# Performance work log

Measured on AMD Instinct MI355X. Metric: run time of the kernel, lower is better.

The kernel has to match this reference:

```python
import jax, jax.numpy as jnp
import numpy as np

N_GRAPH = 100000
N_CAND = 1000
N_EDGES = 3200000
F_IN = 32


def _param(k, shape):
    return jax.random.normal(k, shape, dtype=jnp.float32) * 0.1


def setup_inputs() -> dict:
    key = jax.random.key(0)
    ks = jax.random.split(key, 20)
    inp = {
        "x": jax.random.normal(ks[0], (N_GRAPH, F_IN), dtype=jnp.float32),
        "candidate_set": jax.random.normal(ks[1], (N_CAND, F_IN), dtype=jnp.float32),
        "edge_index": jax.random.randint(ks[2], (2, N_EDGES), 0, N_GRAPH, dtype=jnp.int32),
        # GCN stack 32 -> 16 -> 24 -> 32
        "W1": _param(ks[3], (F_IN, 16)), "b1": jnp.zeros((16,), jnp.float32),
        "W2": _param(ks[4], (16, 24)),   "b2": jnp.zeros((24,), jnp.float32),
        "W3": _param(ks[5], (24, 32)),   "b3": jnp.zeros((32,), jnp.float32),
        # start-node MLP: 32 -> 16 -> 1
        "Ws1": _param(ks[6], (32, 16)), "bs1": jnp.zeros((16,), jnp.float32),
        "Ws2": _param(ks[7], (16, 1)),  "bs2": jnp.zeros((1,), jnp.float32),
        # end-node MLP: 32 -> 24 -> 1
        "We1": _param(ks[8], (32, 24)), "be1": jnp.zeros((24,), jnp.float32),
        "We2": _param(ks[9], (24, 1)),  "be2": jnp.zeros((1,), jnp.float32),
    }
    return inp


def _relu6(v):
    return jnp.clip(v, 0.0, 6.0)


def _gcn(h, row, col, dinv, W, b, N):
    # PyG GCNConv: h @ W, then D^-1/2 (A+I) D^-1/2 aggregation, then + bias
    h = h @ W
    norm = (dinv[row] * dinv[col])[:, None]
    return jax.ops.segment_sum(h[row] * norm, col, num_segments=N) + b


def reference(x, candidate_set, edge_index, W1, b1, W2, b2, W3, b3,
              Ws1, bs1, Ws2, bs2, We1, be1, We2, be2):
    n_graph = x.shape[0]
    h = jnp.concatenate([x, candidate_set], axis=0)  # [N, F_IN]
    N = h.shape[0]
    sl = jnp.arange(N, dtype=edge_index.dtype)
    row = jnp.concatenate([edge_index[0], sl])  # self-loops appended
    col = jnp.concatenate([edge_index[1], sl])
    deg = jax.ops.segment_sum(jnp.ones(row.shape[0], h.dtype), col, num_segments=N)
    dinv = 1.0 / jnp.sqrt(deg)  # deg >= 1 thanks to self-loops

    for W, b in ((W1, b1), (W2, b2), (W3, b3)):
        h = _gcn(h, row, col, dinv, W, b, N)  # [N, 32] at the end

    # start-node head: softmax over nodes (dim 0)
    start_probs = jax.nn.softmax(_relu6(h @ Ws1 + bs1) @ Ws2 + bs2, axis=0)  # [N,1]
    mask = jnp.ones_like(start_probs).at[n_graph:].set(0.0)  # zero out candidates
    start_probs = start_probs * mask
    start_probs = jnp.where(start_probs == 0.0, 1e-10, start_probs)
    start_probs = start_probs.squeeze()  # [N]
    start_node = jax.random.categorical(jax.random.key(42), jnp.log(start_probs))

    # end-node head
    end_probs = jax.nn.softmax(_relu6(h @ We1 + be1) @ We2 + be2, axis=0)  # [N,1]
    end_probs = end_probs.at[start_node].set(0.0)
    end_probs = jnp.where(end_probs == 0.0, 1e-10, end_probs)
    end_probs = end_probs.squeeze()  # [N]
    end_node = jax.random.categorical(jax.random.key(43), jnp.log(end_probs))

    new_edge = jnp.stack([start_node, end_node]).astype(edge_index.dtype)[:, None]
    edge_index_new = jnp.concatenate([edge_index, new_edge], axis=1)
    return (h, start_probs, end_probs, start_node, end_node, edge_index_new)
```

## Files before the change

kernel.cpp:

```cpp
#include <hip/hip_runtime.h>
#include <math.h>

#define TPB 256
#define BNODES 256
#define EPB 8192
#define SENT (-1)
#define MAXBKT 512
#define STAGE_CAP 14144

typedef _Float16 h8 __attribute__((ext_vector_type(8)));
typedef _Float16 hf;


__device__ __forceinline__ float jax_gumbel(unsigned key, unsigned i) {
  unsigned x0 = 0u, x1 = i;
  unsigned ks0 = 0u, ks1 = key, ks2 = key ^ 0x1BD11BDAu;
  x0 += ks0; x1 += ks1;
#define TFR(r) { x0 += x1; x1 = (x1 << (r)) | (x1 >> (32 - (r))); x1 ^= x0; }
  TFR(13) TFR(15) TFR(26) TFR(6)
  x0 += ks1; x1 += ks2 + 1u;
  TFR(17) TFR(29) TFR(16) TFR(24)
  x0 += ks2; x1 += ks0 + 2u;
  TFR(13) TFR(15) TFR(26) TFR(6)
  x0 += ks0; x1 += ks1 + 3u;
  TFR(17) TFR(29) TFR(16) TFR(24)
  x0 += ks1; x1 += ks2 + 4u;
  TFR(13) TFR(15) TFR(26) TFR(6)
  x0 += ks2; x1 += ks0 + 5u;
#undef TFR
  unsigned bits = x0 ^ x1;
  float f = __uint_as_float((bits >> 9) | 0x3f800000u) - 1.0f;
  float u = (f == 0.0f) ? 1.17549435e-38f : f;
  return -logf(-logf(u));
}

__global__ void hist_k(const int* __restrict__ col, int* __restrict__ hist,
                       int ne, int nbkt, int nblk) {
  __shared__ int h[1024];
  int t = threadIdx.x;
  for (int i = t; i < nbkt; i += TPB) h[i] = 0;
  __syncthreads();
  int base = blockIdx.x * EPB;
#pragma unroll
  for (int k = 0; k < EPB / TPB; k++) {
    int idx = base + k * TPB + t;
    if (idx < ne) atomicAdd(&h[col[idx] >> 8], 1);
  }
  __syncthreads();
  for (int i = t; i < nbkt; i += TPB) hist[(size_t)i * nblk + blockIdx.x] = h[i];
}

__global__ void breal_k(const int* __restrict__ hist, int* __restrict__ breal, int nblk) {
  int bkt = blockIdx.x;
  int t = threadIdx.x;
  int s = 0;
  for (int b = t; b < nblk; b += TPB) s += hist[(size_t)bkt * nblk + b];
  __shared__ int red[TPB];
  red[t] = s; __syncthreads();
  for (int st = 128; st > 0; st >>= 1) { if (t < st) red[t] += red[t + st]; __syncthreads(); }
  if (t == 0) breal[bkt] = red[0];
}

template <int PAD>
__global__ void scan1_k(const int* __restrict__ a, int* __restrict__ bsums, int n) {
  int t = threadIdx.x;
  int base = blockIdx.x * 1024 + t * 4;
  int s = 0;
#pragma unroll
  for (int k = 0; k < 4; k++) {
    int i = base + k;
    if (i < n) { int v = a[i]; if (PAD) v = (v + 15) & ~15; s += v; }
  }
  __shared__ int red[TPB];
  red[t] = s; __syncthreads();
  for (int st = 128; st > 0; st >>= 1) { if (t < st) red[t] += red[t + st]; __syncthreads(); }
  if (t == 0) bsums[blockIdx.x] = red[0];
}

__global__ void scan_single_k(int* a, int m) {
  __shared__ int sc[TPB];
  int t = threadIdx.x;
  int v[4]; int s = 0;
#pragma unroll
  for (int k = 0; k < 4; k++) { int i = t * 4 + k; v[k] = (i < m) ? a[i] : 0; s += v[k]; }
  sc[t] = s; __syncthreads();
  for (int off = 1; off < TPB; off <<= 1) {
    int add = (t >= off) ? sc[t - off] : 0;
    __syncthreads();
    sc[t] += add;
    __syncthreads();
  }
  int excl = sc[t] - s;
#pragma unroll
  for (int k = 0; k < 4; k++) { int i = t * 4 + k; if (i < m) a[i] = excl; excl += v[k]; }
  if (t == TPB - 1) a[m] = excl;
}

template <int PAD>
__global__ void scan3_k(const int* __restrict__ a, const int* __restrict__ bsums,
                        int* __restrict__ outp, int n, int nb) {
  int t = threadIdx.x;
  int base = blockIdx.x * 1024 + t * 4;
  int v[4]; int tsum = 0;
#pragma unroll
  for (int k = 0; k < 4; k++) {
    int vv = 0;
    if (base + k < n) { vv = a[base + k]; if (PAD) vv = (vv + 15) & ~15; }
    v[k] = vv; tsum += vv;
  }
  __shared__ int sc[TPB];
  sc[t] = tsum; __syncthreads();
  for (int off = 1; off < TPB; off <<= 1) {
    int add = (t >= off) ? sc[t - off] : 0;
    __syncthreads();
    sc[t] += add;
    __syncthreads();
  }
  int excl = sc[t] - tsum + bsums[blockIdx.x];
#pragma unroll
  for (int k = 0; k < 4; k++) { if (base + k < n) outp[base + k] = excl; excl += v[k]; }
  if (blockIdx.x == 0 && t == 0) outp[n] = bsums[nb];
}

__global__ void __launch_bounds__(TPB, 1)
bscatter_k(const int* __restrict__ row, const int* __restrict__ col,
           const int* __restrict__ histP, int* __restrict__ pairs,
           float* __restrict__ e0, float* __restrict__ e1,
           int ne, int nbkt, int nblk) {
  __shared__ int sbase[MAXBKT], lofs[MAXBKT], lcur[MAXBKT], lsz[MAXBKT];
  __shared__ int ssc[TPB];
  __shared__ int stage[STAGE_CAP];
  int t = threadIdx.x;
  int b = blockIdx.x;
  int i0 = 2 * t, i1 = 2 * t + 1;
  int g0 = 0, L0 = 0, g1 = 0, L1 = 0;
  if (i0 < nbkt) { size_t f = (size_t)i0 * nblk + b; g0 = histP[f]; L0 = histP[f + 1] - g0; }
  if (i1 < nbkt) { size_t f = (size_t)i1 * nblk + b; g1 = histP[f]; L1 = histP[f + 1] - g1; }
  int s = L0 + L1;
  ssc[t] = s; __syncthreads();
  for (int off = 1; off < TPB; off <<= 1) {
    int add = (t >= off) ? ssc[t - off] : 0;
    __syncthreads();
    ssc[t] += add;
    __syncthreads();
  }
  int excl = ssc[t] - s;
  if (i0 < nbkt) { sbase[i0] = g0; lofs[i0] = excl; lcur[i0] = excl; lsz[i0] = L0; }
  if (i1 < nbkt) { sbase[i1] = g1; lofs[i1] = excl + L0; lcur[i1] = excl + L0; lsz[i1] = L1; }
  __syncthreads();
  int base0 = b * EPB;
#pragma unroll
  for (int k = 0; k < EPB / TPB; k++) {
    int idx = base0 + k * TPB + t;
    if (idx < ne) {
      int c = col[idx];
      int r = row[idx];
      int p = atomicAdd(&lcur[c >> 8], 1);
      stage[p] = (r << 8) | (c & 255);
      e0[idx] = (float)r;
      e1[idx] = (float)c;
    }
  }
  __syncthreads();
  for (int i = t; i < nbkt; i += TPB) {
    int en = lcur[i], pe = lofs[i] + lsz[i];
    for (int p = en; p < pe; p++) stage[p] = SENT;
  }
  __syncthreads();
  int4* gp = (int4*)pairs;
  const int4* sp = (const int4*)stage;
  for (int i = t; i < nbkt; i += TPB) {
    int gb = sbase[i] >> 2, lb = lofs[i] >> 2, m = lsz[i] >> 2;
    for (int q = 0; q < m; q++) gp[gb + q] = sp[lb + q];
  }
}

__global__ void bbuild_k(const int* __restrict__ pairs, const int* __restrict__ histP,
                         const int* __restrict__ bbase, int nblk, int* __restrict__ rp,
                         float* __restrict__ dinv, int* __restrict__ csr, int n, int ne) {
  int bkt = blockIdx.x;
  int lo = bkt << 8;
  int t = threadIdx.x;
  int pstart = histP[(size_t)bkt * nblk];
  int pend   = histP[(size_t)(bkt + 1) * nblk];
  int rbase  = bbase[bkt];
  __shared__ int cnt[BNODES], sc[BNODES], pos[BNODES];
  cnt[t] = 0; __syncthreads();
  for (int p = pstart + t; p < pend; p += TPB) {
    int e = pairs[p];
    if (e >= 0) atomicAdd(&cnt[e & 255], 1);
  }
  __syncthreads();
  int own = cnt[t];
  sc[t] = own; __syncthreads();
  for (int off = 1; off < BNODES; off <<= 1) {
    int add = (t >= off) ? sc[t - off] : 0;
    __syncthreads();
    sc[t] += add;
    __syncthreads();
  }
  int excl = sc[t] - own;
  if (lo + t < n) {
    rp[lo + t] = rbase + excl;
    dinv[lo + t] = 1.0f / sqrtf((float)(own + 1));
  }
  pos[t] = rbase + excl;
  __syncthreads();
  for (int p = pstart + t; p < pend; p += TPB) {
    int e = pairs[p];
    if (e >= 0) {
      int q = atomicAdd(&pos[e & 255], 1);
      csr[q] = e >> 8;
    }
  }
  if (bkt == 0 && t == 0) rp[n] = ne;
}

__global__ void prep_k(const float* __restrict__ W2, const float* __restrict__ W3,
                       const float* __restrict__ b1, const float* __restrict__ b2,
                       float* __restrict__ W23, float* __restrict__ bvA, float* __restrict__ bvB) {
  int t = threadIdx.x;
  for (int idx = t; idx < 512; idx += TPB) {
    int i = idx >> 5, j = idx & 31;
    float s = 0.f;
    for (int k = 0; k < 24; k++) s += W2[i * 24 + k] * W3[k * 32 + j];
    W23[idx] = s;
  }
  __syncthreads();
  if (t < 32) {
    float sA = 0.f;
    for (int i = 0; i < 16; i++) sA += b1[i] * W23[i * 32 + t];
    bvA[t] = sA;
    float sB = 0.f;
    for (int k = 0; k < 24; k++) sB += b2[k] * W3[k * 32 + t];
    bvB[t] = sB;
  }
}

__global__ void gemm16h_k(const float* __restrict__ A, const float* __restrict__ A2, int nsplit,
                          const float* __restrict__ W, const float* __restrict__ dinv,
                          hf* __restrict__ out, int n) {
  constexpr int FIN = 32, FOUT = 16, FP = 16;
  constexpr int NODES = TPB / FP;
  __shared__ float Ws[FIN * FOUT];
  __shared__ float Hs[NODES * (FIN + 1)];
  int t = threadIdx.x;
  int base = blockIdx.x * NODES;
  for (int i = t; i < FIN * FOUT; i += TPB) Ws[i] = W[i];
  for (int i = t; i < NODES * FIN; i += TPB) {
    int nl = i / FIN, k = i - nl * FIN;
    int g = base + nl;
    float v = 0.f;
    if (g < n) v = (g < nsplit) ? A[(size_t)g * FIN + k] : A2[(size_t)(g - nsplit) * FIN + k];
    Hs[nl * (FIN + 1) + k] = v;
  }
  __syncthreads();
  int nl = t / FP, j = t % FP;
  int g = base + nl;
  if (g < n) {
    float acc = 0.f;
#pragma unroll
    for (int k = 0; k < FIN; k++) acc += Hs[nl * (FIN + 1) + k] * Ws[k * FOUT + j];
    out[(size_t)g * FOUT + j] = (hf)(acc * dinv[g]);
  }
}

__global__ void agghs_k(const h8* __restrict__ ts, const int* __restrict__ csr,
                        const int* __restrict__ rp, const float* __restrict__ dinv,
                        const float* __restrict__ sin_, float* __restrict__ u_out,
                        float* __restrict__ us_out, h8* __restrict__ outv, int n) {
  int wave = blockIdx.x * (TPB / 64) + (threadIdx.x >> 6);
  int lane = threadIdx.x & 63;
  int j = lane & 1;
  int grp = (lane >> 1) & 3;
  int nl = lane >> 3;
  int c = wave * 8 + nl;
  bool valid = (c < n);
  float acc[8] = {0.f, 0.f, 0.f, 0.f, 0.f, 0.f, 0.f, 0.f};
  float accS = 0.f;
  if (valid) {
    int s = rp[c], e = rp[c + 1];
    int ch0 = s >> 2, ch1 = (e + 3) >> 2;
    int nch = ch1 - ch0;
    int k0 = ch0 + ((nch * grp) >> 2);
    int k1 = ch0 + ((nch * (grp + 1)) >> 2);
    for (int ch = k0; ch < k1; ch++) {
      int base = ch << 2;
      int4 e4 = *(const int4*)(csr + base);
      bool b0 = (base     >= s) & (base     < e);
      bool b1 = (base + 1 >= s) & (base + 1 < e);
      bool b2 = (base + 2 >= s) & (base + 2 < e);
      bool b3 = (base + 3 >= s) & (base + 3 < e);
      int r0 = b0 ? e4.x : 0;
      int r1 = b1 ? e4.y : 0;
      int r2 = b2 ? e4.z : 0;
      int r3 = b3 ? e4.w : 0;
      float m0 = b0 ? 1.f : 0.f, m1 = b1 ? 1.f : 0.f;
      float m2 = b2 ? 1.f : 0.f, m3 = b3 ? 1.f : 0.f;
      h8 v0 = ts[(r0 << 1) | j];
      h8 v1 = ts[(r1 << 1) | j];
      h8 v2 = ts[(r2 << 1) | j];
      h8 v3 = ts[(r3 << 1) | j];
      float sA = sin_[j ? r2 : r0];
      float sB = sin_[j ? r3 : r1];
      accS += sA * (j ? m2 : m0) + sB * (j ? m3 : m1);
#pragma unroll
      for (int k = 0; k < 8; k++)
        acc[k] += m0 * (float)v0[k] + m1 * (float)v1[k] + m2 * (float)v2[k] + m3 * (float)v3[k];
    }
  }
  accS += __shfl_xor(accS, 1, 64);
#pragma unroll
  for (int off = 2; off <= 4; off <<= 1) {
#pragma unroll
    for (int k = 0; k < 8; k++) acc[k] += __shfl_xor(acc[k], off, 64);
    accS += __shfl_xor(accS, off, 64);
  }
  if (valid && grp == 0) {
    h8 self = ts[(c << 1) | j];
    float d = dinv[c];
    float scl = d * d;
    h8 o;
#pragma unroll
    for (int k = 0; k < 8; k++) o[k] = (hf)(scl * (acc[k] + (float)self[k]));
    outv[(c << 1) | j] = o;
    if (j == 0) {
      float u = d * (accS + sin_[c]);
      u_out[c] = u;
      if (us_out) us_out[c] = u * d;
    }
  }
}

__global__ void agghc_k(const h8* __restrict__ ts, const int* __restrict__ csr,
                        const int* __restrict__ rp, const float* __restrict__ dinv,
                        const float* __restrict__ a1, const float* __restrict__ a2,
                        const float* __restrict__ W23, const float* __restrict__ bvA,
                        const float* __restrict__ bvB, const float* __restrict__ b3,
                        float* __restrict__ out, int n) {
  __shared__ float Ws[512], vA[32], vB[32], vb[32];
  __shared__ float t3s[32][17];
  int t = threadIdx.x;
  for (int i = t; i < 512; i += TPB) Ws[i] = W23[i];
  if (t < 32) { vA[t] = bvA[t]; vB[t] = bvB[t]; vb[t] = b3[t]; }
  int wave = t >> 6;
  int lane = t & 63;
  int j = lane & 1;
  int grp = (lane >> 1) & 3;
  int nl = lane >> 3;
  int nlb = wave * 8 + nl;
  int c = blockIdx.x * 32 + nlb;
  bool valid = (c < n);
  float acc[8] = {0.f, 0.f, 0.f, 0.f, 0.f, 0.f, 0.f, 0.f};
  if (valid) {
    int s = rp[c], e = rp[c + 1];
    int ch0 = s >> 2, ch1 = (e + 3) >> 2;
    int nch = ch1 - ch0;
    int k0 = ch0 + ((nch * grp) >> 2);
    int k1 = ch0 + ((nch * (grp + 1)) >> 2);
    for (int ch = k0; ch < k1; ch++) {
      int base = ch << 2;
      int4 e4 = *(const int4*)(csr + base);
      bool b0 = (base     >= s) & (base     < e);
      bool b1 = (base + 1 >= s) & (base + 1 < e);
      bool b2 = (base + 2 >= s) & (base + 2 < e);
      bool b3b = (base + 3 >= s) & (base + 3 < e);
      int r0 = b0 ? e4.x : 0;
      int r1 = b1 ? e4.y : 0;
      int r2 = b2 ? e4.z : 0;
      int r3 = b3b ? e4.w : 0;
      float m0 = b0 ? 1.f : 0.f, m1 = b1 ? 1.f : 0.f;
      float m2 = b2 ? 1.f : 0.f, m3 = b3b ? 1.f : 0.f;
      h8 v0 = ts[(r0 << 1) | j];
      h8 v1 = ts[(r1 << 1) | j];
      h8 v2 = ts[(r2 << 1) | j];
      h8 v3 = ts[(r3 << 1) | j];
#pragma unroll
      for (int k = 0; k < 8; k++)
        acc[k] += m0 * (float)v0[k] + m1 * (float)v1[k] + m2 * (float)v2[k] + m3 * (float)v3[k];
    }
  }
#pragma unroll
  for (int off = 2; off <= 4; off <<= 1) {
#pragma unroll
    for (int k = 0; k < 8; k++) acc[k] += __shfl_xor(acc[k], off, 64);
  }
  if (valid && grp == 0) {
    h8 self = ts[(c << 1) | j];
    float d = dinv[c];
#pragma unroll
    for (int k = 0; k < 8; k++) t3s[nlb][j * 8 + k] = d * (acc[k] + (float)self[k]);
  }
  __syncthreads();
  int n2 = t >> 3, jb = t & 7;
  int g = blockIdx.x * 32 + n2;
  if (g < n) {
    float av = a1[g], bv = a2[g];
#pragma unroll
    for (int q = 0; q < 4; q++) {
      int j2 = jb + q * 8;
      float acc2 = 0.f;
#pragma unroll
      for (int k = 0; k < 16; k++) acc2 += t3s[n2][k] * Ws[k * 32 + j2];
      out[(size_t)g * 32 + j2] = acc2 + bv * vA[j2] + av * vB[j2] + vb[j2];
    }
  }
}

__global__ void __launch_bounds__(TPB, 2)
heads_k(const float* __restrict__ h3,
        const float* __restrict__ Ws1, const float* __restrict__ bs1,
        const float* __restrict__ ws2, const float* __restrict__ bs2,
        const float* __restrict__ We1, const float* __restrict__ be1,
        const float* __restrict__ we2, const float* __restrict__ be2,
        float* __restrict__ slog, float* __restrict__ elog,
        float* __restrict__ pm, int n) {
  __shared__ float W1s[32 * 16], W2s[32 * 24], b1s[16], b2s[24], v1s[16], v2s[24];
  __shared__ float Hs[TPB][33];
  int t = threadIdx.x;
  for (int i = t; i < 32 * 16; i += TPB) W1s[i] = Ws1[i];
  for (int i = t; i < 32 * 24; i += TPB) W2s[i] = We1[i];
  if (t < 16) { b1s[t] = bs1[t]; v1s[t] = ws2[t]; }
  if (t < 24) { b2s[t] = be1[t]; v2s[t] = we2[t]; }
  int rb = blockIdx.x * TPB;
  int nrow = n - rb; if (nrow > TPB) nrow = TPB; if (nrow < 0) nrow = 0;
  const float4* hp = (const float4*)(h3 + (size_t)rb * 32);
  for (int i = t; i < nrow * 8; i += TPB) {
    float4 v = hp[i];
    int rr = i >> 3, cc = (i & 7) << 2;
    Hs[rr][cc] = v.x; Hs[rr][cc + 1] = v.y; Hs[rr][cc + 2] = v.z; Hs[rr][cc + 3] = v.w;
  }
  __syncthreads();
  int i = rb + t;
  float s = -3.402823466e+38f, e2 = -3.402823466e+38f;
  if (i < n) {
    float row[32];
#pragma unroll
    for (int k = 0; k < 32; k++) row[k] = Hs[t][k];
    s = bs2[0];
#pragma unroll
    for (int j = 0; j < 16; j++) {
      float a = b1s[j];
#pragma unroll
      for (int k = 0; k < 32; k++) a += row[k] * W1s[k * 16 + j];
      a = fminf(fmaxf(a, 0.f), 6.f);
      s += a * v1s[j];
    }
    e2 = be2[0];
#pragma unroll
    for (int j = 0; j < 24; j++) {
      float a = b2s[j];
#pragma unroll
      for (int k = 0; k < 32; k++) a += row[k] * W2s[k * 24 + j];
      a = fminf(fmaxf(a, 0.f), 6.f);
      e2 += a * v2s[j];
    }
    slog[i] = s;
    elog[i] = e2;
  }
  __shared__ float sm1[TPB], ss1[TPB], sm2[TPB], ss2[TPB];
  sm1[t] = s;  ss1[t] = (i < n) ? 1.f : 0.f;
  sm2[t] = e2; ss2[t] = (i < n) ? 1.f : 0.f;
  __syncthreads();
  for (int st = 128; st > 0; st >>= 1) {
    if (t < st) {
      float M = fmaxf(sm1[t], sm1[t + st]);
      ss1[t] = ss1[t] * expf(sm1[t] - M) + ss1[t + st] * expf(sm1[t + st] - M);
      sm1[t] = M;
      float M2 = fmaxf(sm2[t], sm2[t + st]);
      ss2[t] = ss2[t] * expf(sm2[t] - M2) + ss2[t + st] * expf(sm2[t + st] - M2);
      sm2[t] = M2;
    }
    __syncthreads();
  }
  if (t == 0) {
    pm[blockIdx.x] = sm1[0]; pm[512 + blockIdx.x] = ss1[0];
    pm[1024 + blockIdx.x] = sm2[0]; pm[1536 + blockIdx.x] = ss2[0];
  }
}

__global__ void osm_fin_k(const float* __restrict__ pm, float* __restrict__ fsc, int nb) {
  int t = threadIdx.x;
  float m1 = -3.402823466e+38f, s1 = 0.f, m2 = -3.402823466e+38f, s2 = 0.f;
  for (int i = t; i < nb; i += TPB) {
    float bm1 = pm[i], bs1v = pm[512 + i];
    float M = fmaxf(m1, bm1);
    s1 = s1 * expf(m1 - M) + bs1v * expf(bm1 - M); m1 = M;
    float bm2 = pm[1024 + i], bs2v = pm[1536 + i];
    float M2 = fmaxf(m2, bm2);
    s2 = s2 * expf(m2 - M2) + bs2v * expf(bm2 - M2); m2 = M2;
  }
  __shared__ float sm1[TPB], ss1[TPB], sm2[TPB], ss2[TPB];
  sm1[t] = m1; ss1[t] = s1; sm2[t] = m2; ss2[t] = s2; __syncthreads();
  for (int st = 128; st > 0; st >>= 1) {
    if (t < st) {
      float M = fmaxf(sm1[t], sm1[t + st]);
      ss1[t] = ss1[t] * expf(sm1[t] - M) + ss1[t + st] * expf(sm1[t + st] - M);
      sm1[t] = M;
      float M2 = fmaxf(sm2[t], sm2[t + st]);
      ss2[t] = ss2[t] * expf(sm2[t] - M2) + ss2[t + st] * expf(sm2[t + st] - M2);
      sm2[t] = M2;
    }
    __syncthreads();
  }
  if (t == 0) { fsc[0] = sm1[0]; fsc[2] = ss1[0]; fsc[1] = sm2[0]; fsc[3] = ss2[0]; }
}

template <int HEAD>
__global__ void pargmax_k(const float* __restrict__ logit, const float* __restrict__ fsc,
                          const int* __restrict__ isc, float* __restrict__ outp,
                          unsigned key, int n, int ngraph, float* pval, int* pidx) {
  int t = threadIdx.x;
  float mx = fsc[HEAD], sm = fsc[2 + HEAD];
  int ban = HEAD ? isc[0] : -1;
  float bv = -3.402823466e+38f;
  int bi = 0x7fffffff;
  for (int i = blockIdx.x * TPB + t; i < n; i += gridDim.x * TPB) {
    float p = expf(logit[i] - mx) / sm;
    if (HEAD == 0) { if (i >= ngraph) p = 0.f; }
    else           { if (i == ban) p = 0.f; }
    if (p == 0.f) p = 1e-10f;
    outp[i] = p;
    float v = logf(p) + jax_gumbel(key, (unsigned)i);
    if (v > bv) { bv = v; bi = i; }
  }
  __shared__ float sv[TPB]; __shared__ int si[TPB];
  sv[t] = bv; si[t] = bi; __syncthreads();
  for (int st = 128; st > 0; st >>= 1) {
    if (t < st) {
      float v2 = sv[t + st]; int i2 = si[t + st];
      if (v2 > sv[t] || (v2 == sv[t] && i2 < si[t])) { sv[t] = v2; si[t] = i2; }
    }
    __syncthreads();
  }
  if (t == 0) { pval[blockIdx.x] = sv[0]; pidx[blockIdx.x] = si[0]; }
}

__global__ void argmax_fin_k(const float* pval, const int* pidx, int nb,
                             int* isc, float* dnode) {
  int t = threadIdx.x;
  float bv = (t < nb) ? pval[t] : -3.402823466e+38f;
  int bi = (t < nb) ? pidx[t] : 0x7fffffff;
  __shared__ float sv[TPB]; __shared__ int si[TPB];
  sv[t] = bv; si[t] = bi; __syncthreads();
  for (int st = 128; st > 0; st >>= 1) {
    if (t < st) {
      float v2 = sv[t + st]; int i2 = si[t + st];
      if (v2 > sv[t] || (v2 == sv[t] && i2 < si[t])) { sv[t] = v2; si[t] = i2; }
    }
    __syncthreads();
  }
  if (t == 0) { isc[0] = si[0]; dnode[0] = (float)si[0]; }
}

__global__ void argmax_fin_end_k(const float* pval, const int* pidx, int nb,
                                 const int* isc, float* p_end, float* p_e0, float* p_e1) {
  int t = threadIdx.x;
  float bv = (t < nb) ? pval[t] : -3.402823466e+38f;
  int bi = (t < nb) ? pidx[t] : 0x7fffffff;
  __shared__ float sv[TPB]; __shared__ int si[TPB];
  sv[t] = bv; si[t] = bi; __syncthreads();
  for (int st = 128; st > 0; st >>= 1) {
    if (t < st) {
      float v2 = sv[t + st]; int i2 = si[t + st];
      if (v2 > sv[t] || (v2 == sv[t] && i2 < si[t])) { sv[t] = v2; si[t] = i2; }
    }
    __syncthreads();
  }
  if (t == 0) {
    int en = si[0];
    p_end[0] = (float)en;
    p_e0[0] = (float)isc[0];
    p_e1[0] = (float)en;
  }
}

extern "C" void kernel_launch(void* const* d_in, const int* in_sizes, int n_in,
                              void* d_out, int out_size, void* d_ws, size_t ws_size,
                              hipStream_t stream) {
  const float* x    = (const float*)d_in[0];
  const float* cand = (const float*)d_in[1];
  const int*   ei   = (const int*)d_in[2];
  const float* W1 = (const float*)d_in[3];  const float* b1  = (const float*)d_in[4];
  const float* W2 = (const float*)d_in[5];  const float* b2  = (const float*)d_in[6];
  const float* W3 = (const float*)d_in[7];  const float* b3  = (const float*)d_in[8];
  const float* Ws1= (const float*)d_in[9];  const float* bs1 = (const float*)d_in[10];
  const float* Ws2= (const float*)d_in[11]; const float* bs2 = (const float*)d_in[12];
  const float* We1= (const float*)d_in[13]; const float* be1 = (const float*)d_in[14];
  const float* We2= (const float*)d_in[15]; const float* be2 = (const float*)d_in[16];

  const int nG = in_sizes[0] / 32, nC = in_sizes[1] / 32;
  const int n  = nG + nC;
  const int ne = in_sizes[2] / 2;

  float* out = (float*)d_out;
  const size_t OFF1 = (size_t)n * 32;
  const size_t OFF2 = OFF1 + n;
  const size_t OFF3 = OFF2 + n;
  const size_t OFF4 = OFF3 + 1;
  const size_t OFF5 = OFF4 + 1;

  const int NBKT = (n + BNODES - 1) / BNODES;
  const int NBLK = (ne + EPB - 1) / EPB;
  const int H    = NBKT * NBLK;
  const int nbh  = (H + 1023) / 1024;

  float* wf = (float*)d_ws;
  int*   wi = (int*)d_ws;
  size_t NP = (((size_t)n + 2) + 63) & ~(size_t)63;
  size_t o = 0;
  int*   rp    = wi + o; o += NP;
  int*   bsums = wi + o; o += 384;
  int*   breal = wi + o; o += 512;
  float* dinv  = wf + o; o += NP;
  float* a1v   = wf + o; o += NP;
  float* a1s   = wf + o; o += NP;
  float* a2v   = wf + o; o += NP;
  float* w23   = wf + o; o += 512;
  float* bvA   = wf + o; o += 64;
  float* bvB   = wf + o; o += 64;
  float* slogv = wf + o; o += NP;
  float* elogv = wf + o; o += NP;
  float* pmA   = wf + o; o += 2048;
  float* aval  = wf + o; o += 512;
  int*   aidx  = wi + o; o += 512;
  float* fsc   = wf + o; o += 64;
  int*   isc   = wi + o; o += 64;
  hf*    hh0   = (hf*)(wf + o); o += (size_t)n * 8 + 64;
  hf*    hh1   = (hf*)(wf + o); o += (size_t)n * 8 + 64;
  int*   hist  = wi + o; o += (size_t)H + 64;
  int*   csr   = wi + o; o += (size_t)ne + 64;
  int*   pairs = wi + o; o += (size_t)ne + 15 * (size_t)H + 64;

  const int* row = ei;
  const int* col = ei + ne;

  int gN = (n + TPB - 1) / TPB;

  hist_k<<<NBLK, TPB, 0, stream>>>(col, hist, ne, NBKT, NBLK);
  breal_k<<<NBKT, TPB, 0, stream>>>(hist, breal, NBLK);
  scan_single_k<<<1, TPB, 0, stream>>>(breal, NBKT);
  scan1_k<1><<<nbh, TPB, 0, stream>>>(hist, bsums, H);
  scan_single_k<<<1, TPB, 0, stream>>>(bsums, nbh);
  scan3_k<1><<<nbh, TPB, 0, stream>>>(hist, bsums, hist, H, nbh);
  bscatter_k<<<NBLK, TPB, 0, stream>>>(row, col, hist, pairs,
                                       out + OFF5, out + OFF5 + ne + 1, ne, NBKT, NBLK);
  bbuild_k<<<NBKT, TPB, 0, stream>>>(pairs, hist, breal, NBLK, rp, dinv, csr, n, ne);

  prep_k<<<1, TPB, 0, stream>>>(W2, W3, b1, b2, w23, bvA, bvB);
  gemm16h_k<<<(n + 15) / 16, TPB, 0, stream>>>(x, cand, nG, W1, dinv, hh0, n);
  int gH = (n + 31) / 32;
  agghs_k<<<gH, TPB, 0, stream>>>((const h8*)hh0, csr, rp, dinv, dinv, a1v, a1s, (h8*)hh1, n);
  agghs_k<<<gH, TPB, 0, stream>>>((const h8*)hh1, csr, rp, dinv, a1s, a2v, nullptr, (h8*)hh0, n);
  agghc_k<<<gH, TPB, 0, stream>>>((const h8*)hh0, csr, rp, dinv, a1v, a2v,
                                  w23, bvA, bvB, b3, out, n);

  heads_k<<<gN, TPB, 0, stream>>>(out, Ws1, bs1, Ws2, bs2, We1, be1, We2, be2,
                                  slogv, elogv, pmA, n);
  osm_fin_k<<<1, TPB, 0, stream>>>(pmA, fsc, gN);

  pargmax_k<0><<<256, TPB, 0, stream>>>(slogv, fsc, nullptr, out + OFF1, 42u, n, nG, aval, aidx);
  argmax_fin_k<<<1, TPB, 0, stream>>>(aval, aidx, 256, isc, out + OFF3);

  pargmax_k<1><<<256, TPB, 0, stream>>>(elogv, fsc, isc, out + OFF2, 43u, n, nG, aval + 256, aidx + 256);
  argmax_fin_end_k<<<1, TPB, 0, stream>>>(aval + 256, aidx + 256, 256, isc,
                                          out + OFF4, out + OFF5 + ne, out + OFF5 + 2 * (size_t)ne + 1);
}
```

Measured before the change: 349.5 us.

## Replace per-block histogram scans with atomic bucket cursors and fuse heads into aggregation

The CSR build drops the per-(bucket,block) histogram and its multi-kernel scan. It now uses a single global bucket count, a one-block scan that reserves padded space, and per-block atomic claims on bucket cursors inside the scatter kernel, which now counts its own local histogram. The start/end MLP heads and the partial softmax reduction are fused into the last aggregation kernel, so the separate heads pass that re-reads h3 from global memory is gone. The cost is extra slack space in the pairs buffer, non-deterministic ordering of edges within a bucket, more shared memory in the fused kernel, and a scatter kernel that reads col twice.

```diff
diff --git a/kernel.cpp b/kernel.cpp
--- a/kernel.cpp
+++ b/kernel.cpp
@@ -6,7 +6,8 @@
 #define EPB 8192
 #define SENT (-1)
 #define MAXBKT 512
-#define STAGE_CAP 14144
+#define STAGE_CAP 9472
+#define PMS 3200
 
 typedef _Float16 h8 __attribute__((ext_vector_type(8)));
 typedef _Float16 hf;
@@ -34,9 +35,32 @@
   return -logf(-logf(u));
 }
 
-__global__ void hist_k(const int* __restrict__ col, int* __restrict__ hist,
-                       int ne, int nbkt, int nblk) {
-  __shared__ int h[1024];
+__global__ void prep_k(const float* __restrict__ W2, const float* __restrict__ W3,
+                       const float* __restrict__ b1, const float* __restrict__ b2,
+                       float* __restrict__ W23, float* __restrict__ bvA, float* __restrict__ bvB,
+                       int* __restrict__ breal, int nbkt) {
+  int t = threadIdx.x;
+  for (int i = t; i < nbkt; i += TPB) breal[i] = 0;
+  for (int idx = t; idx < 512; idx += TPB) {
+    int i = idx >> 5, j = idx & 31;
+    float s = 0.f;
+    for (int k = 0; k < 24; k++) s += W2[i * 24 + k] * W3[k * 32 + j];
+    W23[idx] = s;
+  }
+  __syncthreads();
+  if (t < 32) {
+    float sA = 0.f;
+    for (int i = 0; i < 16; i++) sA += b1[i] * W23[i * 32 + t];
+    bvA[t] = sA;
+    float sB = 0.f;
+    for (int k = 0; k < 24; k++) sB += b2[k] * W3[k * 32 + t];
+    bvB[t] = sB;
+  }
+}
+
+__global__ void hist2_k(const int* __restrict__ col, int* __restrict__ breal,
+                        int ne, int nbkt) {
+  __shared__ int h[MAXBKT];
   int t = threadIdx.x;
   for (int i = t; i < nbkt; i += TPB) h[i] = 0;
   __syncthreads();
@@ -47,108 +71,76 @@
     if (idx < ne) atomicAdd(&h[col[idx] >> 8], 1);
   }
   __syncthreads();
-  for (int i = t; i < nbkt; i += TPB) hist[(size_t)i * nblk + blockIdx.x] = h[i];
-}
-
-__global__ void breal_k(const int* __restrict__ hist, int* __restrict__ breal, int nblk) {
-  int bkt = blockIdx.x;
-  int t = threadIdx.x;
-  int s = 0;
-  for (int b = t; b < nblk; b += TPB) s += hist[(size_t)bkt * nblk + b];
-  __shared__ int red[TPB];
-  red[t] = s; __syncthreads();
-  for (int st = 128; st > 0; st >>= 1) { if (t < st) red[t] += red[t + st]; __syncthreads(); }
-  if (t == 0) breal[bkt] = red[0];
-}
-
-template <int PAD>
-__global__ void scan1_k(const int* __restrict__ a, int* __restrict__ bsums, int n) {
-  int t = threadIdx.x;
-  int base = blockIdx.x * 1024 + t * 4;
-  int s = 0;
-#pragma unroll
-  for (int k = 0; k < 4; k++) {
-    int i = base + k;
-    if (i < n) { int v = a[i]; if (PAD) v = (v + 15) & ~15; s += v; }
-  }
-  __shared__ int red[TPB];
-  red[t] = s; __syncthreads();
-  for (int st = 128; st > 0; st >>= 1) { if (t < st) red[t] += red[t + st]; __syncthreads(); }
-  if (t == 0) bsums[blockIdx.x] = red[0];
-}
-
-__global__ void scan_single_k(int* a, int m) {
-  __shared__ int sc[TPB];
-  int t = threadIdx.x;
-  int v[4]; int s = 0;
-#pragma unroll
-  for (int k = 0; k < 4; k++) { int i = t * 4 + k; v[k] = (i < m) ? a[i] : 0; s += v[k]; }
-  sc[t] = s; __syncthreads();
+  for (int i = t; i < nbkt; i += TPB) if (h[i]) atomicAdd(&breal[i], h[i]);
+}
+
+__global__ void sbase_k(const int* __restrict__ breal, int* __restrict__ rbase,
+                        int* __restrict__ base, int* __restrict__ cursor,
+                        int nbkt, int nblk) {
+  __shared__ int sr[TPB], sp[TPB];
+  int t = threadIdx.x;
+  int vr[2], vp[2]; int tr = 0, tp = 0;
+#pragma unroll
+  for (int k = 0; k < 2; k++) {
+    int i = t * 2 + k; int R = 0, P = 0;
+    if (i < nbkt) {
+      R = breal[i];
+      int mn = (nblk < R) ? nblk : R;
+      P = (R + 3 * mn + 15) & ~15;
+    }
+    vr[k] = R; vp[k] = P; tr += R; tp += P;
+  }
+  sr[t] = tr; sp[t] = tp; __syncthreads();
   for (int off = 1; off < TPB; off <<= 1) {
-    int add = (t >= off) ? sc[t - off] : 0;
-    __syncthreads();
-    sc[t] += add;
-    __syncthreads();
-  }
-  int excl = sc[t] - s;
-#pragma unroll
-  for (int k = 0; k < 4; k++) { int i = t * 4 + k; if (i < m) a[i] = excl; excl += v[k]; }
-  if (t == TPB - 1) a[m] = excl;
-}
-
-template <int PAD>
-__global__ void scan3_k(const int* __restrict__ a, const int* __restrict__ bsums,
-                        int* __restrict__ outp, int n, int nb) {
-  int t = threadIdx.x;
-  int base = blockIdx.x * 1024 + t * 4;
-  int v[4]; int tsum = 0;
-#pragma unroll
-  for (int k = 0; k < 4; k++) {
-    int vv = 0;
-    if (base + k < n) { vv = a[base + k]; if (PAD) vv = (vv + 15) & ~15; }
-    v[k] = vv; tsum += vv;
-  }
-  __shared__ int sc[TPB];
-  sc[t] = tsum; __syncthreads();
-  for (int off = 1; off < TPB; off <<= 1) {
-    int add = (t >= off) ? sc[t - off] : 0;
-    __syncthreads();
-    sc[t] += add;
-    __syncthreads();
-  }
-  int excl = sc[t] - tsum + bsums[blockIdx.x];
-#pragma unroll
-  for (int k = 0; k < 4; k++) { if (base + k < n) outp[base + k] = excl; excl += v[k]; }
-  if (blockIdx.x == 0 && t == 0) outp[n] = bsums[nb];
+    int ar = (t >= off) ? sr[t - off] : 0;
+    int ap = (t >= off) ? sp[t - off] : 0;
+    __syncthreads();
+    sr[t] += ar; sp[t] += ap;
+    __syncthreads();
+  }
+  int er = sr[t] - tr, ep = sp[t] - tp;
+#pragma unroll
+  for (int k = 0; k < 2; k++) {
+    int i = t * 2 + k;
+    if (i < nbkt) { rbase[i] = er; base[i] = ep; cursor[i] = ep; }
+    er += vr[k]; ep += vp[k];
+  }
 }
 
 __global__ void __launch_bounds__(TPB, 1)
-bscatter_k(const int* __restrict__ row, const int* __restrict__ col,
-           const int* __restrict__ histP, int* __restrict__ pairs,
-           float* __restrict__ e0, float* __restrict__ e1,
-           int ne, int nbkt, int nblk) {
+scat_k(const int* __restrict__ row, const int* __restrict__ col,
+       int* __restrict__ cursor, int* __restrict__ pairs,
+       float* __restrict__ e0, float* __restrict__ e1,
+       int ne, int nbkt) {
   __shared__ int sbase[MAXBKT], lofs[MAXBKT], lcur[MAXBKT], lsz[MAXBKT];
   __shared__ int ssc[TPB];
   __shared__ int stage[STAGE_CAP];
   int t = threadIdx.x;
   int b = blockIdx.x;
+  for (int i = t; i < nbkt; i += TPB) lsz[i] = 0;
+  __syncthreads();
+  int base0 = b * EPB;
+#pragma unroll
+  for (int k = 0; k < EPB / TPB; k++) {
+    int idx = base0 + k * TPB + t;
+    if (idx < ne) atomicAdd(&lsz[col[idx] >> 8], 1);
+  }
+  __syncthreads();
   int i0 = 2 * t, i1 = 2 * t + 1;
-  int g0 = 0, L0 = 0, g1 = 0, L1 = 0;
-  if (i0 < nbkt) { size_t f = (size_t)i0 * nblk + b; g0 = histP[f]; L0 = histP[f + 1] - g0; }
-  if (i1 < nbkt) { size_t f = (size_t)i1 * nblk + b; g1 = histP[f]; L1 = histP[f + 1] - g1; }
-  int s = L0 + L1;
+  int L0 = (i0 < nbkt) ? lsz[i0] : 0, L1 = (i1 < nbkt) ? lsz[i1] : 0;
+  int P0 = (L0 + 3) & ~3, P1 = (L1 + 3) & ~3;
+  int s = P0 + P1;
   ssc[t] = s; __syncthreads();
   for (int off = 1; off < TPB; off <<= 1) {
-    int add = (t >= off) ? ssc[t - off] : 0;
-    __syncthreads();
-    ssc[t] += add;
+    int a = (t >= off) ? ssc[t - off] : 0;
+    __syncthreads();
+    ssc[t] += a;
     __syncthreads();
   }
   int excl = ssc[t] - s;
-  if (i0 < nbkt) { sbase[i0] = g0; lofs[i0] = excl; lcur[i0] = excl; lsz[i0] = L0; }
-  if (i1 < nbkt) { sbase[i1] = g1; lofs[i1] = excl + L0; lcur[i1] = excl + L0; lsz[i1] = L1; }
-  __syncthreads();
-  int base0 = b * EPB;
+  if (i0 < nbkt) { lofs[i0] = excl; lcur[i0] = excl; if (L0) sbase[i0] = atomicAdd(&cursor[i0], P0); }
+  if (i1 < nbkt) { lofs[i1] = excl + P0; lcur[i1] = excl + P0; if (L1) sbase[i1] = atomicAdd(&cursor[i1], P1); }
+  __syncthreads();
 #pragma unroll
   for (int k = 0; k < EPB / TPB; k++) {
     int idx = base0 + k * TPB + t;
@@ -163,27 +155,29 @@
   }
   __syncthreads();
   for (int i = t; i < nbkt; i += TPB) {
-    int en = lcur[i], pe = lofs[i] + lsz[i];
+    int en = lofs[i] + lsz[i], pe = lofs[i] + ((lsz[i] + 3) & ~3);
     for (int p = en; p < pe; p++) stage[p] = SENT;
   }
   __syncthreads();
   int4* gp = (int4*)pairs;
   const int4* sp = (const int4*)stage;
   for (int i = t; i < nbkt; i += TPB) {
-    int gb = sbase[i] >> 2, lb = lofs[i] >> 2, m = lsz[i] >> 2;
+    int L = lsz[i]; if (!L) continue;
+    int gb = sbase[i] >> 2, lb = lofs[i] >> 2, m = ((L + 3) & ~3) >> 2;
     for (int q = 0; q < m; q++) gp[gb + q] = sp[lb + q];
   }
 }
 
-__global__ void bbuild_k(const int* __restrict__ pairs, const int* __restrict__ histP,
-                         const int* __restrict__ bbase, int nblk, int* __restrict__ rp,
-                         float* __restrict__ dinv, int* __restrict__ csr, int n, int ne) {
+__global__ void bbuild_k(const int* __restrict__ pairs, const int* __restrict__ base,
+                         const int* __restrict__ cursor, const int* __restrict__ rbase,
+                         int* __restrict__ rp, float* __restrict__ dinv,
+                         int* __restrict__ csr, int n, int ne) {
   int bkt = blockIdx.x;
   int lo = bkt << 8;
   int t = threadIdx.x;
-  int pstart = histP[(size_t)bkt * nblk];
-  int pend   = histP[(size_t)(bkt + 1) * nblk];
-  int rbase  = bbase[bkt];
+  int pstart = base[bkt];
+  int pend   = cursor[bkt];
+  int rbase_ = rbase[bkt];
   __shared__ int cnt[BNODES], sc[BNODES], pos[BNODES];
   cnt[t] = 0; __syncthreads();
   for (int p = pstart + t; p < pend; p += TPB) {
@@ -201,10 +195,10 @@
   }
   int excl = sc[t] - own;
   if (lo + t < n) {
-    rp[lo + t] = rbase + excl;
+    rp[lo + t] = rbase_ + excl;
     dinv[lo + t] = 1.0f / sqrtf((float)(own + 1));
   }
-  pos[t] = rbase + excl;
+  pos[t] = rbase_ + excl;
   __syncthreads();
   for (int p = pstart + t; p < pend; p += TPB) {
     int e = pairs[p];
@@ -214,27 +208,6 @@
     }
   }
   if (bkt == 0 && t == 0) rp[n] = ne;
-}
-
-__global__ void prep_k(const float* __restrict__ W2, const float* __restrict__ W3,
-                       const float* __restrict__ b1, const float* __restrict__ b2,
-                       float* __restrict__ W23, float* __restrict__ bvA, float* __restrict__ bvB) {
-  int t = threadIdx.x;
-  for (int idx = t; idx < 512; idx += TPB) {
-    int i = idx >> 5, j = idx & 31;
-    float s = 0.f;
-    for (int k = 0; k < 24; k++) s += W2[i * 24 + k] * W3[k * 32 + j];
-    W23[idx] = s;
-  }
-  __syncthreads();
-  if (t < 32) {
-    float sA = 0.f;
-    for (int i = 0; i < 16; i++) sA += b1[i] * W23[i * 32 + t];
-    bvA[t] = sA;
-    float sB = 0.f;
-    for (int k = 0; k < 24; k++) sB += b2[k] * W3[k * 32 + t];
-    bvB[t] = sB;
-  }
 }
 
 __global__ void gemm16h_k(const float* __restrict__ A, const float* __restrict__ A2, int nsplit,
@@ -332,17 +305,29 @@
   }
 }
 
-__global__ void agghc_k(const h8* __restrict__ ts, const int* __restrict__ csr,
-                        const int* __restrict__ rp, const float* __restrict__ dinv,
-                        const float* __restrict__ a1, const float* __restrict__ a2,
-                        const float* __restrict__ W23, const float* __restrict__ bvA,
-                        const float* __restrict__ bvB, const float* __restrict__ b3,
-                        float* __restrict__ out, int n) {
+__global__ void agghch_k(const h8* __restrict__ ts, const int* __restrict__ csr,
+                         const int* __restrict__ rp, const float* __restrict__ dinv,
+                         const float* __restrict__ a1, const float* __restrict__ a2,
+                         const float* __restrict__ W23, const float* __restrict__ bvA,
+                         const float* __restrict__ bvB, const float* __restrict__ b3,
+                         const float* __restrict__ Ws1, const float* __restrict__ bs1,
+                         const float* __restrict__ ws2, const float* __restrict__ bs2,
+                         const float* __restrict__ We1, const float* __restrict__ be1,
+                         const float* __restrict__ we2, const float* __restrict__ be2,
+                         float* __restrict__ out, float* __restrict__ slog,
+                         float* __restrict__ elog, float* __restrict__ pm, int n) {
   __shared__ float Ws[512], vA[32], vB[32], vb[32];
   __shared__ float t3s[32][17];
-  int t = threadIdx.x;
-  for (int i = t; i < 512; i += TPB) Ws[i] = W23[i];
+  __shared__ float h3s[32][33];
+  __shared__ float W1s[512], W2s[768], b1s[16], b2s[24], v1s[16], v2s[24], sb2[2];
+  __shared__ float sm1[32], su1[32], sm2[32], su2[32];
+  int t = threadIdx.x;
+  for (int i = t; i < 512; i += TPB) { Ws[i] = W23[i]; W1s[i] = Ws1[i]; }
+  for (int i = t; i < 768; i += TPB) W2s[i] = We1[i];
   if (t < 32) { vA[t] = bvA[t]; vB[t] = bvB[t]; vb[t] = b3[t]; }
+  if (t < 16) { b1s[t] = bs1[t]; v1s[t] = ws2[t]; }
+  if (t < 24) { b2s[t] = be1[t]; v2s[t] = we2[t]; }
+  if (t == 0) { sb2[0] = bs2[0]; sb2[1] = be2[0]; }
   int wave = t >> 6;
   int lane = t & 63;
   int j = lane & 1;
@@ -402,80 +387,62 @@
       float acc2 = 0.f;
 #pragma unroll
       for (int k = 0; k < 16; k++) acc2 += t3s[n2][k] * Ws[k * 32 + j2];
-      out[(size_t)g * 32 + j2] = acc2 + bv * vA[j2] + av * vB[j2] + vb[j2];
-    }
-  }
-}
-
-__global__ void __launch_bounds__(TPB, 2)
-heads_k(const float* __restrict__ h3,
-        const float* __restrict__ Ws1, const float* __restrict__ bs1,
-        const float* __restrict__ ws2, const float* __restrict__ bs2,
-        const float* __restrict__ We1, const float* __restrict__ be1,
-        const float* __restrict__ we2, const float* __restrict__ be2,
-        float* __restrict__ slog, float* __restrict__ elog,
-        float* __restrict__ pm, int n) {
-  __shared__ float W1s[32 * 16], W2s[32 * 24], b1s[16], b2s[24], v1s[16], v2s[24];
-  __shared__ float Hs[TPB][33];
-  int t = threadIdx.x;
-  for (int i = t; i < 32 * 16; i += TPB) W1s[i] = Ws1[i];
-  for (int i = t; i < 32 * 24; i += TPB) W2s[i] = We1[i];
-  if (t < 16) { b1s[t] = bs1[t]; v1s[t] = ws2[t]; }
-  if (t < 24) { b2s[t] = be1[t]; v2s[t] = we2[t]; }
-  int rb = blockIdx.x * TPB;
-  int nrow = n - rb; if (nrow > TPB) nrow = TPB; if (nrow < 0) nrow = 0;
-  const float4* hp = (const float4*)(h3 + (size_t)rb * 32);
-  for (int i = t; i < nrow * 8; i += TPB) {
-    float4 v = hp[i];
-    int rr = i >> 3, cc = (i & 7) << 2;
-    Hs[rr][cc] = v.x; Hs[rr][cc + 1] = v.y; Hs[rr][cc + 2] = v.z; Hs[rr][cc + 3] = v.w;
-  }
-  __syncthreads();
-  int i = rb + t;
-  float s = -3.402823466e+38f, e2 = -3.402823466e+38f;
-  if (i < n) {
-    float row[32];
-#pragma unroll
-    for (int k = 0; k < 32; k++) row[k] = Hs[t][k];
-    s = bs2[0];
-#pragma unroll
-    for (int j = 0; j < 16; j++) {
-      float a = b1s[j];
-#pragma unroll
-      for (int k = 0; k < 32; k++) a += row[k] * W1s[k * 16 + j];
+      float hv = acc2 + bv * vA[j2] + av * vB[j2] + vb[j2];
+      out[(size_t)g * 32 + j2] = hv;
+      h3s[n2][j2] = hv;
+    }
+  }
+  __syncthreads();
+  float sP = 0.f, eP = 0.f;
+  if (g < n) {
+#pragma unroll
+    for (int jj = 0; jj < 16; jj += 8) {
+      int jh = jj + jb;
+      float a = b1s[jh];
+#pragma unroll
+      for (int k = 0; k < 32; k++) a += h3s[n2][k] * W1s[k * 16 + jh];
       a = fminf(fmaxf(a, 0.f), 6.f);
-      s += a * v1s[j];
-    }
-    e2 = be2[0];
-#pragma unroll
-    for (int j = 0; j < 24; j++) {
-      float a = b2s[j];
-#pragma unroll
-      for (int k = 0; k < 32; k++) a += row[k] * W2s[k * 24 + j];
+      sP += a * v1s[jh];
+    }
+#pragma unroll
+    for (int jj = 0; jj < 24; jj += 8) {
+      int jh = jj + jb;
+      float a = b2s[jh];
+#pragma unroll
+      for (int k = 0; k < 32; k++) a += h3s[n2][k] * W2s[k * 24 + jh];
       a = fminf(fmaxf(a, 0.f), 6.f);
-      e2 += a * v2s[j];
-    }
-    slog[i] = s;
-    elog[i] = e2;
-  }
-  __shared__ float sm1[TPB], ss1[TPB], sm2[TPB], ss2[TPB];
-  sm1[t] = s;  ss1[t] = (i < n) ? 1.f : 0.f;
-  sm2[t] = e2; ss2[t] = (i < n) ? 1.f : 0.f;
-  __syncthreads();
-  for (int st = 128; st > 0; st >>= 1) {
+      eP += a * v2s[jh];
+    }
+  }
+#pragma unroll
+  for (int off = 1; off <= 4; off <<= 1) {
+    sP += __shfl_xor(sP, off, 64);
+    eP += __shfl_xor(eP, off, 64);
+  }
+  if (jb == 0) {
+    float s = -3.402823466e+38f, e2 = -3.402823466e+38f, w = 0.f;
+    if (g < n) {
+      s = sP + sb2[0]; e2 = eP + sb2[1]; w = 1.f;
+      slog[g] = s; elog[g] = e2;
+    }
+    sm1[n2] = s;  su1[n2] = w;
+    sm2[n2] = e2; su2[n2] = w;
+  }
+  __syncthreads();
+  for (int st = 16; st > 0; st >>= 1) {
     if (t < st) {
       float M = fmaxf(sm1[t], sm1[t + st]);
-      ss1[t] = ss1[t] * expf(sm1[t] - M) + ss1[t + st] * expf(sm1[t + st] - M);
+      su1[t] = su1[t] * expf(sm1[t] - M) + su1[t + st] * expf(sm1[t + st] - M);
       sm1[t] = M;
       float M2 = fmaxf(sm2[t], sm2[t + st]);
-      ss2[t] = ss2[t] * expf(sm2[t] - M2) + ss2[t + st] * expf(sm2[t + st] - M2);
+      su2[t] = su2[t] * expf(sm2[t] - M2) + su2[t + st] * expf(sm2[t + st] - M2);
       sm2[t] = M2;
     }
     __syncthreads();
   }
   if (t == 0) {
-    pm[blockIdx.x] = sm1[0]; pm[512 + blockIdx.x] = ss1[0];
-    pm[1024 + blockIdx.x] = sm2[0]; pm[1536 + blockIdx.x] = ss2[0];
+    pm[blockIdx.x] = sm1[0]; pm[PMS + blockIdx.x] = su1[0];
+    pm[2 * PMS + blockIdx.x] = sm2[0]; pm[3 * PMS + blockIdx.x] = su2[0];
   }
 }
 
@@ -483,10 +450,10 @@
   int t = threadIdx.x;
   float m1 = -3.402823466e+38f, s1 = 0.f, m2 = -3.402823466e+38f, s2 = 0.f;
   for (int i = t; i < nb; i += TPB) {
-    float bm1 = pm[i], bs1v = pm[512 + i];
+    float bm1 = pm[i], bs1v = pm[PMS + i];
     float M = fmaxf(m1, bm1);
     s1 = s1 * expf(m1 - M) + bs1v * expf(bm1 - M); m1 = M;
-    float bm2 = pm[1024 + i], bs2v = pm[1536 + i];
+    float bm2 = pm[2 * PMS + i], bs2v = pm[3 * PMS + i];
     float M2 = fmaxf(m2, bm2);
     s2 = s2 * expf(m2 - M2) + bs2v * expf(bm2 - M2); m2 = M2;
   }
@@ -602,16 +569,16 @@
 
   const int NBKT = (n + BNODES - 1) / BNODES;
   const int NBLK = (ne + EPB - 1) / EPB;
-  const int H    = NBKT * NBLK;
-  const int nbh  = (H + 1023) / 1024;
 
   float* wf = (float*)d_ws;
   int*   wi = (int*)d_ws;
   size_t NP = (((size_t)n + 2) + 63) & ~(size_t)63;
   size_t o = 0;
   int*   rp    = wi + o; o += NP;
-  int*   bsums = wi + o; o += 384;
   int*   breal = wi + o; o += 512;
+  int*   rbase = wi + o; o += 512;
+  int*   bbase = wi + o; o += 512;
+  int*   bcur  = wi + o; o += 512;
   float* dinv  = wf + o; o += NP;
   float* a1v   = wf + o; o += NP;
   float* a1s   = wf + o; o += NP;
@@ -621,43 +588,35 @@
   float* bvB   = wf + o; o += 64;
   float* slogv = wf + o; o += NP;
   float* elogv = wf + o; o += NP;
-  float* pmA   = wf + o; o += 2048;
+  float* pmA   = wf + o; o += 4 * PMS;
   float* aval  = wf + o; o += 512;
   int*   aidx  = wi + o; o += 512;
   float* fsc   = wf + o; o += 64;
   int*   isc   = wi + o; o += 64;
   hf*    hh0   = (hf*)(wf + o); o += (size_t)n * 8 + 64;
   hf*    hh1   = (hf*)(wf + o); o += (size_t)n * 8 + 64;
-  int*   hist  = wi + o; o += (size_t)H + 64;
   int*   csr   = wi + o; o += (size_t)ne + 64;
-  int*   pairs = wi + o; o += (size_t)ne + 15 * (size_t)H + 64;
+  int*   pairs = wi + o; o += (size_t)ne + 700000;
 
   const int* row = ei;
   const int* col = ei + ne;
 
-  int gN = (n + TPB - 1) / TPB;
-
-  hist_k<<<NBLK, TPB, 0, stream>>>(col, hist, ne, NBKT, NBLK);
-  breal_k<<<NBKT, TPB, 0, stream>>>(hist, breal, NBLK);
-  scan_single_k<<<1, TPB, 0, stream>>>(breal, NBKT);
-  scan1_k<1><<<nbh, TPB, 0, stream>>>(hist, bsums, H);
-  scan_single_k<<<1, TPB, 0, stream>>>(bsums, nbh);
-  scan3_k<1><<<nbh, TPB, 0, stream>>>(hist, bsums, hist, H, nbh);
-  bscatter_k<<<NBLK, TPB, 0, stream>>>(row, col, hist, pairs,
-                                       out + OFF5, out + OFF5 + ne + 1, ne, NBKT, NBLK);
-  bbuild_k<<<NBKT, TPB, 0, stream>>>(pairs, hist, breal, NBLK, rp, dinv, csr, n, ne);
-
-  prep_k<<<1, TPB, 0, stream>>>(W2, W3, b1, b2, w23, bvA, bvB);
+  prep_k<<<1, TPB, 0, stream>>>(W2, W3, b1, b2, w23, bvA, bvB, breal, NBKT);
+  hist2_k<<<NBLK, TPB, 0, stream>>>(col, breal, ne, NBKT);
+  sbase_k<<<1, TPB, 0, stream>>>(breal, rbase, bbase, bcur, NBKT, NBLK);
+  scat_k<<<NBLK, TPB, 0, stream>>>(row, col, bcur, pairs,
+                                   out + OFF5, out + OFF5 + ne + 1, ne, NBKT);
+  bbuild_k<<<NBKT, TPB, 0, stream>>>(pairs, bbase, bcur, rbase, rp, dinv, csr, n, ne);
+
   gemm16h_k<<<(n + 15) / 16, TPB, 0, stream>>>(x, cand, nG, W1, dinv, hh0, n);
   int gH = (n + 31) / 32;
   agghs_k<<<gH, TPB, 0, stream>>>((const h8*)hh0, csr, rp, dinv, dinv, a1v, a1s, (h8*)hh1, n);
   agghs_k<<<gH, TPB, 0, stream>>>((const h8*)hh1, csr, rp, dinv, a1s, a2v, nullptr, (h8*)hh0, n);
-  agghc_k<<<gH, TPB, 0, stream>>>((const h8*)hh0, csr, rp, dinv, a1v, a2v,
-                                  w23, bvA, bvB, b3, out, n);
-
-  heads_k<<<gN, TPB, 0, stream>>>(out, Ws1, bs1, Ws2, bs2, We1, be1, We2, be2,
-                                  slogv, elogv, pmA, n);
-  osm_fin_k<<<1, TPB, 0, stream>>>(pmA, fsc, gN);
+  agghch_k<<<gH, TPB, 0, stream>>>((const h8*)hh0, csr, rp, dinv, a1v, a2v,
+                                   w23, bvA, bvB, b3,
+                                   Ws1, bs1, Ws2, bs2, We1, be1, We2, be2,
+                                   out, slogv, elogv, pmA, n);
+  osm_fin_k<<<1, TPB, 0, stream>>>(pmA, fsc, gH);
 
   pargmax_k<0><<<256, TPB, 0, stream>>>(slogv, fsc, nullptr, out + OFF1, 42u, n, nG, aval, aidx);
   argmax_fin_k<<<1, TPB, 0, stream>>>(aval, aidx, 256, isc, out + OFF3);
```

New measurement: 345.8 us. About the same (-1.1%).
